# Kernel optimization log

Hardware: AMD Instinct MI355X
Metric: run time of the kernel (lower is better)

## Reference

```python
import jax, jax.numpy as jnp
import numpy as np
from jax import lax

B, CI, CO, H, W = 2, 256, 256, 128, 128
K = 3
K2 = K * K  # 9 kernel taps
BN_EPS = 1e-5


def setup_inputs() -> dict:
    key = jax.random.key(0)
    ks = jax.random.split(key, 9)
    x = jax.random.normal(ks[0], (B, CI, H, W), jnp.float32)
    # conv_offset_mask: Conv2d(chi, 3*K2, 3, stride=1, pad=1) -> [o_y/o_x interleaved (2*K2) | mask (K2)]
    w_off = jax.random.normal(ks[1], (3 * K2, CI, K, K), jnp.float32) * 0.01
    b_off = jax.random.normal(ks[2], (3 * K2,), jnp.float32) * 0.01
    # modulated deformable conv weight/bias
    w_dcn = jax.random.normal(ks[3], (CO, CI, K, K), jnp.float32) * (1.0 / np.float32(np.sqrt(CI * K2)))
    b_dcn = jax.random.normal(ks[4], (CO,), jnp.float32) * 0.01
    # BatchNorm2d (eval-mode affine + running stats)
    gamma = jax.random.uniform(ks[5], (CO,), jnp.float32, 0.5, 1.5)
    beta = jax.random.normal(ks[6], (CO,), jnp.float32) * 0.1
    run_mean = jax.random.normal(ks[7], (CO,), jnp.float32) * 0.1
    run_var = jax.random.uniform(ks[8], (CO,), jnp.float32, 0.5, 1.5)
    return {"x": x, "w_off": w_off, "b_off": b_off, "w_dcn": w_dcn,
            "b_dcn": b_dcn, "gamma": gamma, "beta": beta,
            "run_mean": run_mean, "run_var": run_var}


def _bilinear(x, py, px):
    """Sample x [B,C,H,W] at fractional coords (py,px) [B,H,W]; zero outside."""
    Bx, C, Hx, Wx = x.shape
    y0 = jnp.floor(py)
    x0 = jnp.floor(px)
    ly = py - y0
    lx = px - x0
    xf = x.reshape(Bx, C, Hx * Wx)

    def gather(yy, xx):
        valid = ((yy >= 0) & (yy <= Hx - 1) & (xx >= 0) & (xx <= Wx - 1)).astype(x.dtype)
        yi = jnp.clip(yy, 0, Hx - 1).astype(jnp.int32)
        xi = jnp.clip(xx, 0, Wx - 1).astype(jnp.int32)
        idx = (yi * Wx + xi).reshape(Bx, 1, Hx * Wx)
        v = jnp.take_along_axis(xf, idx, axis=2).reshape(Bx, C, Hx, Wx)
        return v * valid[:, None]

    w00 = ((1 - ly) * (1 - lx))[:, None]
    w01 = ((1 - ly) * lx)[:, None]
    w10 = (ly * (1 - lx))[:, None]
    w11 = (ly * lx)[:, None]
    return (w00 * gather(y0, x0) + w01 * gather(y0, x0 + 1)
            + w10 * gather(y0 + 1, x0) + w11 * gather(y0 + 1, x0 + 1))


def _deform_conv_bn_relu(x, w_off, b_off, w_dcn, b_dcn, gamma, beta, run_mean, run_var):
    # offset/mask predictor conv (stride 1, pad 1)
    om = lax.conv_general_dilated(x, w_off, (1, 1), ((1, 1), (1, 1))) + b_off[None, :, None, None]
    dy = om[:, 0:2 * K2:2]          # [B,K2,H,W]
    dx = om[:, 1:2 * K2:2]          # [B,K2,H,W]
    mask = jax.nn.sigmoid(om[:, 2 * K2:])  # [B,K2,H,W] modulation

    hh = jnp.arange(H, dtype=x.dtype)[:, None]  # [H,1]
    ww = jnp.arange(W, dtype=x.dtype)[None, :]  # [1,W]

    out = jnp.zeros((x.shape[0], w_dcn.shape[0], H, W), x.dtype)
    for k in range(K2):  # fixed small loop over the 9 kernel taps
        i, j = k // K, k % K
        py = hh - 1 + i + dy[:, k]  # pad=1, dilation=1
        px = ww - 1 + j + dx[:, k]
        val = _bilinear(x, py, px) * mask[:, k][:, None]  # [B,CI,H,W]
        out = out + jnp.einsum('oc,bchw->bohw', w_dcn[:, :, i, j], val)
    out = out + b_dcn[None, :, None, None]

    # BatchNorm2d (eval mode) + ReLU
    inv = gamma / jnp.sqrt(run_var + BN_EPS)
    out = out * inv[None, :, None, None] + (beta - run_mean * inv)[None, :, None, None]
    return jnp.maximum(out, 0.0)


def reference(x, w_off, b_off, w_dcn, b_dcn, gamma, beta, run_mean, run_var):
    return _deform_conv_bn_relu(x, w_off, b_off, w_dcn, b_dcn, gamma, beta, run_mean, run_var)
```

## Files before the change

### kernel.cpp

```cpp
#include <hip/hip_runtime.h>
#include <math.h>

#define Bn 2
#define CIc 256
#define COc 256
#define Hh 128
#define Ww 128
#define HW (Hh*Ww)

typedef unsigned short u16;
typedef unsigned int u32;
typedef __bf16 bf16x8 __attribute__((ext_vector_type(8)));
typedef float  f32x4  __attribute__((ext_vector_type(4)));
typedef float  f32x2  __attribute__((ext_vector_type(2)));
typedef u32    u32x4v __attribute__((ext_vector_type(4)));

#define WOFP_OFF  0
#define WPACK_OFF 36864
#define SCALE_OFF 331776
#define SHIFT_OFF 332032
#define XT_OFF    332288

__device__ __forceinline__ u16 f2bf(float f) {
    u32 u = __builtin_bit_cast(u32, f);
    return (u16)((u + 0x7FFFu + ((u >> 16) & 1u)) >> 16);
}
__device__ __forceinline__ u32 pkbf(float lo, float hi) {
    __bf16 a = (__bf16)lo, b = (__bf16)hi;
    return (u32)__builtin_bit_cast(u16, a) | ((u32)__builtin_bit_cast(u16, b) << 16);
}
__device__ __forceinline__ f32x2 unpk(u32 u) {
    f32x2 r;
    r.x = __builtin_bit_cast(float, u << 16);
    r.y = __builtin_bit_cast(float, u & 0xFFFF0000u);
    return r;
}

__global__ void prep_kernel(const float* __restrict__ w_off,
                            const float* __restrict__ w_dcn,
                            const float* __restrict__ b_dcn,
                            const float* __restrict__ gamma,
                            const float* __restrict__ beta,
                            const float* __restrict__ rmean,
                            const float* __restrict__ rvar,
                            float* __restrict__ ws) {
    int tid = blockIdx.x*blockDim.x + threadIdx.x;
    int nth = gridDim.x*blockDim.x;
    u16* wofp = (u16*)(ws + WOFP_OFF);
    u16* wpk  = (u16*)(ws + WPACK_OFF);
    for (int idx = tid; idx < 9*8*32*4*8; idx += nth) {
        int j = idx & 7, kb = (idx>>3)&3, co = (idx>>5)&31, s = (idx>>10)&7, k = idx>>13;
        int ci = kb*64 + s*8 + j;
        float v = (co < 27) ? w_off[(co*CIc + ci)*9 + k] : 0.f;
        wofp[idx] = f2bf(v);
    }
    for (int idx = tid; idx < 9*8*256*4*8; idx += nth) {
        int j = idx & 7, kb = (idx>>3)&3, co = (idx>>5)&255, s = (idx>>13)&7, k = idx>>16;
        int ci = kb*64 + s*8 + j;
        wpk[idx] = f2bf(w_dcn[(co*CIc + ci)*9 + k]);
    }
    if (tid < COc) {
        float inv = gamma[tid] * rsqrtf(rvar[tid] + 1e-5f);
        ws[SCALE_OFF+tid] = inv;
        ws[SHIFT_OFF+tid] = beta[tid] - rmean[tid]*inv + b_dcn[tid]*inv;
    }
}

__global__ __launch_bounds__(256) void transpose_kernel(const float* __restrict__ x,
                                                        float* __restrict__ ws) {
    __shared__ float tile[256][33];
    int bid = blockIdx.x;
    int b   = bid >> 9;
    int pxt = bid & 511;
    const float* xb = x + (size_t)b*CIc*HW + pxt*32;
    int px = threadIdx.x & 31, cg = threadIdx.x >> 5;
    #pragma unroll 8
    for (int it = 0; it < 32; it++) {
        int ci = it*8 + cg;
        tile[ci][px] = xb[(size_t)ci*HW + px];
    }
    __syncthreads();
    int px2 = threadIdx.x >> 3, oct = threadIdx.x & 7;
    u16* xto = (u16*)(ws + XT_OFF) + (((size_t)b*HW + pxt*32 + px2) << 8);
    #pragma unroll
    for (int uu = 0; uu < 4; uu++) {
        int u = uu*8 + oct;
        int cib = (u & 3)*64 + (u >> 2)*8;
        u32x4v v;
        #pragma unroll
        for (int t = 0; t < 4; t++)
            v[t] = pkbf(tile[cib + 2*t][px2], tile[cib + 2*t + 1][px2]);
        *(u32x4v*)(xto + u*8) = v;
    }
}

__device__ __forceinline__ void calc_corners(const float* spy, const float* spxs, const float* smk,
        int k, int p_s, int sub, const u16* xt,
        float& w00, float& w01, float& w10, float& w11,
        const u16*& x00, const u16*& x01, const u16*& x10, const u16*& x11) {
    float pyv = spy[k*64 + p_s], pxv = spxs[k*64 + p_s], mv = smk[k*64 + p_s];
    float y0f = floorf(pyv), x0f = floorf(pxv);
    float ly = pyv - y0f, lx = pxv - x0f;
    int y0 = (int)y0f, x0i = (int)x0f;
    int y1 = y0 + 1, x1i = x0i + 1;
    float wy0 = ((unsigned)y0  < Hh) ? (1.f-ly) : 0.f;
    float wy1 = ((unsigned)y1  < Hh) ? ly       : 0.f;
    float wx0 = ((unsigned)x0i < Ww) ? (1.f-lx) : 0.f;
    float wx1 = ((unsigned)x1i < Ww) ? lx       : 0.f;
    w00 = wy0*wx0*mv; w01 = wy0*wx1*mv; w10 = wy1*wx0*mv; w11 = wy1*wx1*mv;
    int cy0 = min(max(y0,0),Hh-1), cy1 = min(max(y1,0),Hh-1);
    int cx0 = min(max(x0i,0),Ww-1), cx1 = min(max(x1i,0),Ww-1);
    x00 = xt + ((((cy0<<7)+cx0)<<8) + sub*8);
    x01 = xt + ((((cy0<<7)+cx1)<<8) + sub*8);
    x10 = xt + ((((cy1<<7)+cx0)<<8) + sub*8);
    x11 = xt + ((((cy1<<7)+cx1)<<8) + sub*8);
}

#define LOADG(gg, ubase) \
    _Pragma("unroll") for (int t = 0; t < 2; t++) { \
        int o = ((ubase) + t) << 5; \
        gg[t][0] = *(const u32x4v*)(x00 + o); \
        gg[t][1] = *(const u32x4v*)(x01 + o); \
        gg[t][2] = *(const u32x4v*)(x10 + o); \
        gg[t][3] = *(const u32x4v*)(x11 + o); \
    }

#define CONSG(gg, ubase, dst) \
    _Pragma("unroll") for (int t = 0; t < 2; t++) { \
        u32x4v vv; \
        _Pragma("unroll") for (int w2 = 0; w2 < 4; w2++) { \
            f32x2 r = unpk(gg[t][0][w2])*w00 + unpk(gg[t][1][w2])*w01 \
                    + unpk(gg[t][2][w2])*w10 + unpk(gg[t][3][w2])*w11; \
            vv[w2] = pkbf(r.x, r.y); \
        } \
        u32 uoff = (((u32)((ubase) + t) << 6) | wsub) ^ wswz; \
        *(u32x4v*)((dst) + wrbase0 + uoff) = vv; \
    }

#define GEMMSTEP(s) { \
    u32 inn = ((u32)((s)*64 + kb*16)) ^ rswz; \
    _Pragma("unroll") for (int bq = 0; bq < 4; bq++) { \
        bf16x8 bb = *(const bf16x8*)(base_r + (pxl + bq*16)*512 + inn); \
        _Pragma("unroll") for (int mi = 0; mi < 4; mi++) \
            acc[mi][bq] = __builtin_amdgcn_mfma_f32_16x16x32_bf16(apre[(s)&1][mi], bb, acc[mi][bq], 0,0,0); \
    } }

#define APREF(ptr) { \
    _Pragma("unroll") for (int mi = 0; mi < 4; mi++) \
        apre[s&1][mi] = *(const bf16x8*)((ptr) + mi*512); }

__global__ __launch_bounds__(256, 2) void fused_kernel(const float* __restrict__ b_off,
                                                       const float* __restrict__ ws,
                                                       float* __restrict__ out) {
    __shared__ __align__(16) char smem[65536 + 3*576*4];
    float* fin  = (float*)smem;
    float* spy  = (float*)(smem + 65536);
    float* spxs = spy + 576;
    float* smk  = spxs + 576;

    int tid = threadIdx.x;
    int bid = blockIdx.x;
    int tile = (bid & 7)*64 + (bid >> 3);
    int b = tile >> 8;
    int pixbase = (tile & 255) * 64;
    int h  = pixbase >> 7;
    int w0 = pixbase & 127;

    const u16* wofp = (const u16*)(ws + WOFP_OFF);
    const u16* wpk  = (const u16*)(ws + WPACK_OFF);
    const u16* xt   = (const u16*)(ws + XT_OFF) + (size_t)b*HW*256;

    int l  = tid & 63;
    int wv = tid >> 6;
    int kb = l >> 4;
    int pxl = l & 15;
    int aoff = pxl*32 + kb*8;

    {
        int pxa = wv*16 + pxl;
        f32x4 oa0 = {0.f,0.f,0.f,0.f}, oa1 = {0.f,0.f,0.f,0.f};
        #pragma unroll
        for (int k = 0; k < 9; k++) {
            int ky = k/3, kx = k - 3*ky;
            int y  = h + ky - 1;
            int xw = w0 + pxa + kx - 1;
            bool ok = ((unsigned)y < Hh) && ((unsigned)xw < Ww);
            const u16* brow = xt + (((y << 7) + xw) << 8);
            const u16* wk = wofp + k*8192;
            bf16x8 bfC = {};
            if (ok) bfC = *(const bf16x8*)(brow + kb*8);
            bf16x8 a0C = *(const bf16x8*)(wk + aoff);
            bf16x8 a1C = *(const bf16x8*)(wk + 512 + aoff);
            #pragma unroll
            for (int s = 0; s < 8; s++) {
                bf16x8 bfN = {}, a0N = {}, a1N = {};
                if (s < 7) {
                    if (ok) bfN = *(const bf16x8*)(brow + (s+1)*32 + kb*8);
                    a0N = *(const bf16x8*)(wk + (s+1)*1024 + aoff);
                    a1N = *(const bf16x8*)(wk + (s+1)*1024 + 512 + aoff);
                }
                oa0 = __builtin_amdgcn_mfma_f32_16x16x32_bf16(a0C, bfC, oa0, 0,0,0);
                oa1 = __builtin_amdgcn_mfma_f32_16x16x32_bf16(a1C, bfC, oa1, 0,0,0);
                if (s < 7) { bfC = bfN; a0C = a0N; a1C = a1N; }
            }
        }
        #pragma unroll
        for (int r = 0; r < 4; r++) {
            fin[(kb*4 + r)*64 + pxa]      = oa0[r];
            fin[(16 + kb*4 + r)*64 + pxa] = oa1[r];
        }
    }
    __syncthreads();
    for (int idx = tid; idx < 576; idx += 256) {
        int k = idx >> 6, p = idx & 63;
        float dy = fin[(2*k)*64 + p]   + b_off[2*k];
        float dx = fin[(2*k+1)*64 + p] + b_off[2*k+1];
        float mv = fin[(18+k)*64 + p]  + b_off[18+k];
        spy[idx]  = (float)(h - 1 + k/3) + dy;
        spxs[idx] = (float)(w0 + p - 1 + k%3) + dx;
        smk[idx]  = 1.f/(1.f + __expf(-mv));
    }
    __syncthreads();

    int p_s = tid >> 2;
    int sub = tid & 3;
    u32 wrbase0 = (u32)p_s*512;
    u32 wsub = (u32)sub << 4;
    u32 wswz = (u32)(p_s & 7) << 4;
    u32 rswz = (u32)(pxl & 7) << 4;

    f32x4 acc[4][4];
    #pragma unroll
    for (int mi = 0; mi < 4; mi++)
        #pragma unroll
        for (int bq = 0; bq < 4; bq++)
            acc[mi][bq] = (f32x4){0.f,0.f,0.f,0.f};

    bf16x8 apre[2][4];

    {
        float w00,w01,w10,w11; const u16 *x00,*x01,*x10,*x11;
        calc_corners(spy, spxs, smk, 0, p_s, sub, xt, w00,w01,w10,w11, x00,x01,x10,x11);
        u32x4v ga[2][4], gb[2][4];
        LOADG(ga, 0); LOADG(gb, 2);
        CONSG(ga, 0, smem); CONSG(gb, 2, smem);
        LOADG(ga, 4); LOADG(gb, 6);
        CONSG(ga, 4, smem); CONSG(gb, 6, smem);
    }
    {
        const u16* ap0 = wpk + wv*2048 + aoff;
        #pragma unroll
        for (int mi = 0; mi < 4; mi++) {
            apre[0][mi] = *(const bf16x8*)(ap0 + mi*512);
            apre[1][mi] = *(const bf16x8*)(ap0 + 8192 + mi*512);
        }
    }
    __syncthreads();

    for (int k = 0; k < 8; k++) {
        const char* base_r = smem + ((k & 1) << 15);
        char* base_w = smem + (((k + 1) & 1) << 15);
        const u16* wkb   = wpk + k*65536 + wv*2048 + aoff;
        const u16* wkb_n = wkb + 65536;

        float w00,w01,w10,w11; const u16 *x00,*x01,*x10,*x11;
        calc_corners(spy, spxs, smk, k+1, p_s, sub, xt, w00,w01,w10,w11, x00,x01,x10,x11);

        u32x4v g0[2][4], g1[2][4];
        #pragma unroll
        for (int s = 0; s < 8; s++) {
            __builtin_amdgcn_sched_barrier(0);
            __builtin_amdgcn_s_setprio(1);
            GEMMSTEP(s);
            __builtin_amdgcn_s_setprio(0);
            { const u16* ap = (s < 6) ? (wkb + (s+2)*8192) : (wkb_n + (s-6)*8192); APREF(ap); }
            if (s == 0) { LOADG(g0, 0); }
            if (s == 1) { LOADG(g1, 2); }
            if (s == 4) { CONSG(g0, 0, base_w); LOADG(g0, 4); }
            if (s == 5) { CONSG(g1, 2, base_w); LOADG(g1, 6); }
            if (s == 7) { CONSG(g0, 4, base_w); }
        }
        CONSG(g1, 6, base_w);
        __syncthreads();
    }
    {
        const char* base_r = smem;
        const u16* wkb = wpk + 8*65536 + wv*2048 + aoff;
        #pragma unroll
        for (int s = 0; s < 8; s++) {
            __builtin_amdgcn_sched_barrier(0);
            __builtin_amdgcn_s_setprio(1);
            GEMMSTEP(s);
            __builtin_amdgcn_s_setprio(0);
            if (s < 6) { const u16* ap = wkb + (s+2)*8192; APREF(ap); }
        }
    }

    int rbase = kb*4;
    #pragma unroll
    for (int mi = 0; mi < 4; mi++) {
        #pragma unroll
        for (int r = 0; r < 4; r++) {
            int co = wv*64 + mi*16 + rbase + r;
            float sc = ws[SCALE_OFF+co], sh = ws[SHIFT_OFF+co];
            float* op = out + ((size_t)(b*COc + co))*HW + pixbase + pxl;
            #pragma unroll
            for (int bq = 0; bq < 4; bq++)
                op[bq*16] = fmaxf(acc[mi][bq][r]*sc + sh, 0.f);
        }
    }
}

extern "C" void kernel_launch(void* const* d_in, const int* in_sizes, int n_in,
                              void* d_out, int out_size, void* d_ws, size_t ws_size,
                              hipStream_t stream) {
    const float* x     = (const float*)d_in[0];
    const float* w_off = (const float*)d_in[1];
    const float* b_off = (const float*)d_in[2];
    const float* w_dcn = (const float*)d_in[3];
    const float* b_dcn = (const float*)d_in[4];
    const float* gamma = (const float*)d_in[5];
    const float* beta  = (const float*)d_in[6];
    const float* rmean = (const float*)d_in[7];
    const float* rvar  = (const float*)d_in[8];
    float* out = (float*)d_out;
    float* ws  = (float*)d_ws;

    prep_kernel<<<512, 256, 0, stream>>>(w_off, w_dcn, b_dcn, gamma, beta, rmean, rvar, ws);
    transpose_kernel<<<1024, 256, 0, stream>>>(x, ws);
    fused_kernel<<<512, 256, 0, stream>>>(b_off, ws, out);
}
```

Baseline: 110.3 us.

## Halve pixel tile to 32 per block for more blocks and occupancy

Each block of the fused kernel now covers 32 output pixels instead of 64, and the grid doubles to 1024 blocks. Shared memory is halved, the accumulator shrinks to 4x2, and launch bounds ask for 3 blocks per CU, all to raise occupancy and fill the GPU better. The gather work is re-split across 8 threads per pixel, and only two waves compute the offset conv, whose manual software prefetch is removed. In exchange, each weight tile is reused over fewer pixels, so the weight reads from L2 roughly double, and two waves sit idle during the offset phase.

```diff
diff --git a/kernel.cpp b/kernel.cpp
--- a/kernel.cpp
+++ b/kernel.cpp
@@ -95,10 +95,10 @@
 }
 
 __device__ __forceinline__ void calc_corners(const float* spy, const float* spxs, const float* smk,
-        int k, int p_s, int sub, const u16* xt,
+        int k, int p_s, int sub8, const u16* xt,
         float& w00, float& w01, float& w10, float& w11,
         const u16*& x00, const u16*& x01, const u16*& x10, const u16*& x11) {
-    float pyv = spy[k*64 + p_s], pxv = spxs[k*64 + p_s], mv = smk[k*64 + p_s];
+    float pyv = spy[k*32 + p_s], pxv = spxs[k*32 + p_s], mv = smk[k*32 + p_s];
     float y0f = floorf(pyv), x0f = floorf(pxv);
     float ly = pyv - y0f, lx = pxv - x0f;
     int y0 = (int)y0f, x0i = (int)x0f;
@@ -110,36 +110,30 @@
     w00 = wy0*wx0*mv; w01 = wy0*wx1*mv; w10 = wy1*wx0*mv; w11 = wy1*wx1*mv;
     int cy0 = min(max(y0,0),Hh-1), cy1 = min(max(y1,0),Hh-1);
     int cx0 = min(max(x0i,0),Ww-1), cx1 = min(max(x1i,0),Ww-1);
-    x00 = xt + ((((cy0<<7)+cx0)<<8) + sub*8);
-    x01 = xt + ((((cy0<<7)+cx1)<<8) + sub*8);
-    x10 = xt + ((((cy1<<7)+cx0)<<8) + sub*8);
-    x11 = xt + ((((cy1<<7)+cx1)<<8) + sub*8);
-}
-
-#define LOADG(gg, ubase) \
-    _Pragma("unroll") for (int t = 0; t < 2; t++) { \
-        int o = ((ubase) + t) << 5; \
-        gg[t][0] = *(const u32x4v*)(x00 + o); \
-        gg[t][1] = *(const u32x4v*)(x01 + o); \
-        gg[t][2] = *(const u32x4v*)(x10 + o); \
-        gg[t][3] = *(const u32x4v*)(x11 + o); \
-    }
-
-#define CONSG(gg, ubase, dst) \
-    _Pragma("unroll") for (int t = 0; t < 2; t++) { \
-        u32x4v vv; \
-        _Pragma("unroll") for (int w2 = 0; w2 < 4; w2++) { \
-            f32x2 r = unpk(gg[t][0][w2])*w00 + unpk(gg[t][1][w2])*w01 \
-                    + unpk(gg[t][2][w2])*w10 + unpk(gg[t][3][w2])*w11; \
-            vv[w2] = pkbf(r.x, r.y); \
-        } \
-        u32 uoff = (((u32)((ubase) + t) << 6) | wsub) ^ wswz; \
-        *(u32x4v*)((dst) + wrbase0 + uoff) = vv; \
-    }
+    x00 = xt + ((((cy0<<7)+cx0)<<8) + sub8*8);
+    x01 = xt + ((((cy0<<7)+cx1)<<8) + sub8*8);
+    x10 = xt + ((((cy1<<7)+cx0)<<8) + sub8*8);
+    x11 = xt + ((((cy1<<7)+cx1)<<8) + sub8*8);
+}
+
+#define LOAD1(gg, u) { \
+    gg[0] = *(const u32x4v*)(x00 + ((u) << 6)); \
+    gg[1] = *(const u32x4v*)(x01 + ((u) << 6)); \
+    gg[2] = *(const u32x4v*)(x10 + ((u) << 6)); \
+    gg[3] = *(const u32x4v*)(x11 + ((u) << 6)); }
+
+#define CONS1(gg, u, dst) { \
+    u32x4v vv; \
+    _Pragma("unroll") for (int w2 = 0; w2 < 4; w2++) { \
+        f32x2 r = unpk(gg[0][w2])*w00 + unpk(gg[1][w2])*w01 \
+                + unpk(gg[2][w2])*w10 + unpk(gg[3][w2])*w11; \
+        vv[w2] = pkbf(r.x, r.y); \
+    } \
+    *(u32x4v*)((dst) + wrbase0 + ((u32)(((u) << 7) | (sub8 << 4)) ^ wswz)) = vv; }
 
 #define GEMMSTEP(s) { \
     u32 inn = ((u32)((s)*64 + kb*16)) ^ rswz; \
-    _Pragma("unroll") for (int bq = 0; bq < 4; bq++) { \
+    _Pragma("unroll") for (int bq = 0; bq < 2; bq++) { \
         bf16x8 bb = *(const bf16x8*)(base_r + (pxl + bq*16)*512 + inn); \
         _Pragma("unroll") for (int mi = 0; mi < 4; mi++) \
             acc[mi][bq] = __builtin_amdgcn_mfma_f32_16x16x32_bf16(apre[(s)&1][mi], bb, acc[mi][bq], 0,0,0); \
@@ -149,20 +143,20 @@
     _Pragma("unroll") for (int mi = 0; mi < 4; mi++) \
         apre[s&1][mi] = *(const bf16x8*)((ptr) + mi*512); }
 
-__global__ __launch_bounds__(256, 2) void fused_kernel(const float* __restrict__ b_off,
+__global__ __launch_bounds__(256, 3) void fused_kernel(const float* __restrict__ b_off,
                                                        const float* __restrict__ ws,
                                                        float* __restrict__ out) {
-    __shared__ __align__(16) char smem[65536 + 3*576*4];
+    __shared__ __align__(16) char smem[32768 + 3*288*4];
     float* fin  = (float*)smem;
-    float* spy  = (float*)(smem + 65536);
-    float* spxs = spy + 576;
-    float* smk  = spxs + 576;
+    float* spy  = (float*)(smem + 32768);
+    float* spxs = spy + 288;
+    float* smk  = spxs + 288;
 
     int tid = threadIdx.x;
     int bid = blockIdx.x;
-    int tile = (bid & 7)*64 + (bid >> 3);
-    int b = tile >> 8;
-    int pixbase = (tile & 255) * 64;
+    int tile = (bid & 7)*128 + (bid >> 3);
+    int b = tile >> 9;
+    int pixbase = (tile & 511) * 32;
     int h  = pixbase >> 7;
     int w0 = pixbase & 127;
 
@@ -176,7 +170,7 @@
     int pxl = l & 15;
     int aoff = pxl*32 + kb*8;
 
-    {
+    if (wv < 2) {
         int pxa = wv*16 + pxl;
         f32x4 oa0 = {0.f,0.f,0.f,0.f}, oa1 = {0.f,0.f,0.f,0.f};
         #pragma unroll
@@ -187,65 +181,58 @@
             bool ok = ((unsigned)y < Hh) && ((unsigned)xw < Ww);
             const u16* brow = xt + (((y << 7) + xw) << 8);
             const u16* wk = wofp + k*8192;
-            bf16x8 bfC = {};
-            if (ok) bfC = *(const bf16x8*)(brow + kb*8);
-            bf16x8 a0C = *(const bf16x8*)(wk + aoff);
-            bf16x8 a1C = *(const bf16x8*)(wk + 512 + aoff);
             #pragma unroll
             for (int s = 0; s < 8; s++) {
-                bf16x8 bfN = {}, a0N = {}, a1N = {};
-                if (s < 7) {
-                    if (ok) bfN = *(const bf16x8*)(brow + (s+1)*32 + kb*8);
-                    a0N = *(const bf16x8*)(wk + (s+1)*1024 + aoff);
-                    a1N = *(const bf16x8*)(wk + (s+1)*1024 + 512 + aoff);
-                }
-                oa0 = __builtin_amdgcn_mfma_f32_16x16x32_bf16(a0C, bfC, oa0, 0,0,0);
-                oa1 = __builtin_amdgcn_mfma_f32_16x16x32_bf16(a1C, bfC, oa1, 0,0,0);
-                if (s < 7) { bfC = bfN; a0C = a0N; a1C = a1N; }
+                bf16x8 bf = {};
+                if (ok) bf = *(const bf16x8*)(brow + s*32 + kb*8);
+                bf16x8 a0 = *(const bf16x8*)(wk + s*1024 + aoff);
+                bf16x8 a1 = *(const bf16x8*)(wk + s*1024 + 512 + aoff);
+                oa0 = __builtin_amdgcn_mfma_f32_16x16x32_bf16(a0, bf, oa0, 0,0,0);
+                oa1 = __builtin_amdgcn_mfma_f32_16x16x32_bf16(a1, bf, oa1, 0,0,0);
             }
         }
         #pragma unroll
         for (int r = 0; r < 4; r++) {
-            fin[(kb*4 + r)*64 + pxa]      = oa0[r];
-            fin[(16 + kb*4 + r)*64 + pxa] = oa1[r];
+            fin[(kb*4 + r)*32 + pxa]      = oa0[r];
+            fin[(16 + kb*4 + r)*32 + pxa] = oa1[r];
         }
     }
     __syncthreads();
-    for (int idx = tid; idx < 576; idx += 256) {
-        int k = idx >> 6, p = idx & 63;
-        float dy = fin[(2*k)*64 + p]   + b_off[2*k];
-        float dx = fin[(2*k+1)*64 + p] + b_off[2*k+1];
-        float mv = fin[(18+k)*64 + p]  + b_off[18+k];
+    for (int idx = tid; idx < 288; idx += 256) {
+        int k = idx >> 5, p = idx & 31;
+        float dy = fin[(2*k)*32 + p]   + b_off[2*k];
+        float dx = fin[(2*k+1)*32 + p] + b_off[2*k+1];
+        float mv = fin[(18+k)*32 + p]  + b_off[18+k];
         spy[idx]  = (float)(h - 1 + k/3) + dy;
         spxs[idx] = (float)(w0 + p - 1 + k%3) + dx;
         smk[idx]  = 1.f/(1.f + __expf(-mv));
     }
     __syncthreads();
 
-    int p_s = tid >> 2;
-    int sub = tid & 3;
+    int p_s = tid >> 3;
+    int sub8 = tid & 7;
     u32 wrbase0 = (u32)p_s*512;
-    u32 wsub = (u32)sub << 4;
     u32 wswz = (u32)(p_s & 7) << 4;
     u32 rswz = (u32)(pxl & 7) << 4;
 
-    f32x4 acc[4][4];
+    f32x4 acc[4][2];
     #pragma unroll
-    for (int mi = 0; mi < 4; mi++)
-        #pragma unroll
-        for (int bq = 0; bq < 4; bq++)
-            acc[mi][bq] = (f32x4){0.f,0.f,0.f,0.f};
+    for (int mi = 0; mi < 4; mi++) {
+        acc[mi][0] = (f32x4){0.f,0.f,0.f,0.f};
+        acc[mi][1] = (f32x4){0.f,0.f,0.f,0.f};
+    }
 
     bf16x8 apre[2][4];
+    u32x4v g0[4], g1[4];
 
     {
         float w00,w01,w10,w11; const u16 *x00,*x01,*x10,*x11;
-        calc_corners(spy, spxs, smk, 0, p_s, sub, xt, w00,w01,w10,w11, x00,x01,x10,x11);
-        u32x4v ga[2][4], gb[2][4];
-        LOADG(ga, 0); LOADG(gb, 2);
-        CONSG(ga, 0, smem); CONSG(gb, 2, smem);
-        LOADG(ga, 4); LOADG(gb, 6);
-        CONSG(ga, 4, smem); CONSG(gb, 6, smem);
+        calc_corners(spy, spxs, smk, 0, p_s, sub8, xt, w00,w01,w10,w11, x00,x01,x10,x11);
+        LOAD1(g0, 0); LOAD1(g1, 1);
+        CONS1(g0, 0, smem); LOAD1(g0, 2);
+        CONS1(g1, 1, smem); LOAD1(g1, 3);
+        CONS1(g0, 2, smem);
+        CONS1(g1, 3, smem);
     }
     {
         const u16* ap0 = wpk + wv*2048 + aoff;
@@ -258,15 +245,14 @@
     __syncthreads();
 
     for (int k = 0; k < 8; k++) {
-        const char* base_r = smem + ((k & 1) << 15);
-        char* base_w = smem + (((k + 1) & 1) << 15);
+        const char* base_r = smem + ((k & 1) << 14);
+        char* base_w = smem + (((k + 1) & 1) << 14);
         const u16* wkb   = wpk + k*65536 + wv*2048 + aoff;
         const u16* wkb_n = wkb + 65536;
 
         float w00,w01,w10,w11; const u16 *x00,*x01,*x10,*x11;
-        calc_corners(spy, spxs, smk, k+1, p_s, sub, xt, w00,w01,w10,w11, x00,x01,x10,x11);
-
-        u32x4v g0[2][4], g1[2][4];
+        calc_corners(spy, spxs, smk, k+1, p_s, sub8, xt, w00,w01,w10,w11, x00,x01,x10,x11);
+
         #pragma unroll
         for (int s = 0; s < 8; s++) {
             __builtin_amdgcn_sched_barrier(0);
@@ -274,13 +260,13 @@
             GEMMSTEP(s);
             __builtin_amdgcn_s_setprio(0);
             { const u16* ap = (s < 6) ? (wkb + (s+2)*8192) : (wkb_n + (s-6)*8192); APREF(ap); }
-            if (s == 0) { LOADG(g0, 0); }
-            if (s == 1) { LOADG(g1, 2); }
-            if (s == 4) { CONSG(g0, 0, base_w); LOADG(g0, 4); }
-            if (s == 5) { CONSG(g1, 2, base_w); LOADG(g1, 6); }
-            if (s == 7) { CONSG(g0, 4, base_w); }
-        }
-        CONSG(g1, 6, base_w);
+            if (s == 0) { LOAD1(g0, 0); }
+            if (s == 1) { LOAD1(g1, 1); }
+            if (s == 4) { CONS1(g0, 0, base_w); LOAD1(g0, 2); }
+            if (s == 5) { CONS1(g1, 1, base_w); LOAD1(g1, 3); }
+            if (s == 7) { CONS1(g0, 2, base_w); }
+        }
+        CONS1(g1, 3, base_w);
         __syncthreads();
     }
     {
@@ -304,9 +290,8 @@
             int co = wv*64 + mi*16 + rbase + r;
             float sc = ws[SCALE_OFF+co], sh = ws[SHIFT_OFF+co];
             float* op = out + ((size_t)(b*COc + co))*HW + pixbase + pxl;
-            #pragma unroll
-            for (int bq = 0; bq < 4; bq++)
-                op[bq*16] = fmaxf(acc[mi][bq][r]*sc + sh, 0.f);
+            op[0]  = fmaxf(acc[mi][0][r]*sc + sh, 0.f);
+            op[16] = fmaxf(acc[mi][1][r]*sc + sh, 0.f);
         }
     }
 }
@@ -328,5 +313,5 @@
 
     prep_kernel<<<512, 256, 0, stream>>>(w_off, w_dcn, b_dcn, gamma, beta, rmean, rvar, ws);
     transpose_kernel<<<1024, 256, 0, stream>>>(x, ws);
-    fused_kernel<<<512, 256, 0, stream>>>(b_off, ws, out);
-}
+    fused_kernel<<<1024, 256, 0, stream>>>(b_off, ws, out);
+}
```

New measurement: 149.1 us. 1.35x slower.
